# Kernel optimization log

Measured on AMD Instinct MI355X. Metric: run time of the kernel, lower is better.

The kernel has to match this reference:

```python
import jax, jax.numpy as jnp
import numpy as np

BINS = 100
MIN, MAX = 0.0, 1.0
DELTA = (MAX - MIN) / BINS
NORM = True
K = 2  # half-window: relu(delta - 0.5*(|dx|+|dy|)) is zero unless |x-c| < 2*delta per axis,
       # and centers are spaced delta apart, so only offsets -2..2 around the containing bin contribute.
BIG = 1e9  # sentinel distance for out-of-range bins -> zero weight


def setup_inputs() -> dict:
    key = jax.random.key(0)
    x = jax.random.uniform(key, (16, 131072, 2), dtype=jnp.float32)  # [B, N, 2] in [0,1)
    return {"x": x}


def reference(x):
    # Faithful to the torch double loop:
    #   counts[b,i,j] = sum_n relu(delta - 0.5*(|x[b,n,0]-c_i| + |x[b,n,1]-c_j|))
    # The triangular kernel has compact support, so each point touches at most a
    # 5x5 neighborhood of bins; compute those weights and scatter-add them.
    B, N, _ = x.shape
    centers = MIN + DELTA * (jnp.arange(BINS, dtype=x.dtype) + 0.5)  # [BINS]
    offs = jnp.arange(-K, K + 1)                                     # [5]

    idx = jnp.floor((x - MIN) / DELTA).astype(jnp.int32)             # [B,N,2] containing bin
    idx = jnp.clip(idx, 0, BINS - 1)
    nb = idx[..., None] + offs                                       # [B,N,2,5] candidate bins
    valid = (nb >= 0) & (nb < BINS)
    nbc = jnp.clip(nb, 0, BINS - 1)

    d = jnp.abs(x[..., None] - centers[nbc])                         # [B,N,2,5] per-axis L1 dist
    d = jnp.where(valid, d, BIG)                                     # kill out-of-range bins

    # combined 5x5 triangular weights per point
    w = jax.nn.relu(DELTA - 0.5 * (d[:, :, 0, :, None] + d[:, :, 1, None, :]))  # [B,N,5,5]

    ii = nbc[:, :, 0, :, None]                                       # [B,N,5,1]
    jj = nbc[:, :, 1, None, :]                                       # [B,N,1,5]
    flat = (jnp.arange(B, dtype=jnp.int32)[:, None, None, None] * (BINS * BINS)
            + ii * BINS + jj)                                        # [B,N,5,5]

    counts = jnp.zeros(B * BINS * BINS, dtype=x.dtype)
    counts = counts.at[flat.reshape(-1)].add(w.reshape(-1))
    counts = counts.reshape(B, BINS, BINS)

    if NORM:
        counts = counts / (counts.sum(axis=(1, 2), keepdims=True) + 1e-5)
    return counts
```

## Files before the change

### kernel.cpp

```cpp
#include <hip/hip_runtime.h>


#define BINS     100
#define NBINS2   (BINS * BINS)
#define NPOINTS  131072
#define NBATCH   16
#define PPB      32
#define CHUNK    (NPOINTS / PPB)
#define THREADS  1024
#define NPART    (NBATCH * PPB)
#define QSCALE   33554432.0f
#define QINV     (1.0 / 33554432.0)

__device__ __forceinline__ void accum_point_q(unsigned* lh, float x0, float x1) {
    int i0 = __float2int_rd(__fmul_rn(x0, 100.0f)); i0 = min(max(i0, 0), BINS - 1);
    int i1 = __float2int_rd(__fmul_rn(x1, 100.0f)); i1 = min(max(i1, 0), BINS - 1);
    const float fi0 = (float)i0, fi1 = (float)i1;
    const float c00 = __fmul_rn(0.01f, fi0 + 0.5f);
    const float c10 = __fmul_rn(0.01f, fi1 + 0.5f);
    const float e00 = fabsf(__fsub_rn(x0, c00));
    const float e10 = fabsf(__fsub_rn(x1, c10));
    float e0m = fabsf(__fsub_rn(x0, __fmul_rn(0.01f, fi0 - 0.5f)));
    float e0p = fabsf(__fsub_rn(x0, __fmul_rn(0.01f, fi0 + 1.5f)));
    float e1m = fabsf(__fsub_rn(x1, __fmul_rn(0.01f, fi1 - 0.5f)));
    float e1p = fabsf(__fsub_rn(x1, __fmul_rn(0.01f, fi1 + 1.5f)));
    e0m = (i0 > 0)        ? e0m : 1e9f;
    e0p = (i0 < BINS - 1) ? e0p : 1e9f;
    e1m = (i1 > 0)        ? e1m : 1e9f;
    e1p = (i1 < BINS - 1) ? e1p : 1e9f;
    const bool up0 = (x0 > c00), up1 = (x1 > c10);
    const int   f0  = up0 ? i0 + 2 : i0 - 2;
    const int   f1  = up1 ? i1 + 2 : i1 - 2;
    const float ff0 = up0 ? fi0 + 2.0f : fi0 - 2.0f;
    const float ff1 = up1 ? fi1 + 2.0f : fi1 - 2.0f;
    float e0f = fabsf(__fsub_rn(x0, __fmul_rn(0.01f, ff0 + 0.5f)));
    float e1f = fabsf(__fsub_rn(x1, __fmul_rn(0.01f, ff1 + 0.5f)));
    e0f = ((unsigned)f0 < (unsigned)BINS) ? e0f : 1e9f;
    e1f = ((unsigned)f1 < (unsigned)BINS) ? e1f : 1e9f;

    const int rm = max(i0 - 1, 0) * BINS;
    const int r0 = i0 * BINS;
    const int rp = min(i0 + 1, BINS - 1) * BINS;
    const int rf = min(max(f0, 0), BINS - 1) * BINS;
    const int cm = max(i1 - 1, 0);
    const int cc = i1;
    const int cp = min(i1 + 1, BINS - 1);
    const int cf = min(max(f1, 0), BINS - 1);

#define SITEU(EA, EB, ADDR) do {                                               \
        const float w_ = fmaxf(fmaf(-0.5f, __fadd_rn(EA, EB), 0.01f), 0.0f);   \
        atomicAdd(&lh[ADDR], (unsigned)fmaf(w_, QSCALE, 0.5f));                \
    } while (0)
#define SITEQ(EA, EB, ADDR) do {                                               \
        const float w_ = fmaf(-0.5f, __fadd_rn(EA, EB), 0.01f);                \
        if (w_ > 0.0f)                                                         \
            atomicAdd(&lh[ADDR], (unsigned)fmaf(w_, QSCALE, 0.5f));            \
    } while (0)
    SITEQ(e0m, e1m, rm + cm); SITEU(e0m, e10, rm + cc); SITEQ(e0m, e1p, rm + cp);
    SITEU(e00, e1m, r0 + cm); SITEU(e00, e10, r0 + cc); SITEU(e00, e1p, r0 + cp);
    SITEQ(e0p, e1m, rp + cm); SITEU(e0p, e10, rp + cc); SITEQ(e0p, e1p, rp + cp);
    SITEQ(e0f, e10, rf + cc);
    SITEQ(e00, e1f, r0 + cf);
#undef SITEU
#undef SITEQ
}

__global__ __launch_bounds__(THREADS) void hist_part_kernel(
    const float* __restrict__ x, unsigned* __restrict__ part,
    unsigned long long* __restrict__ totals)
{
    __shared__ __align__(16) unsigned lh[NBINS2];
    uint4* lh4 = (uint4*)lh;
    for (int i = threadIdx.x; i < NBINS2 / 4; i += THREADS)
        lh4[i] = make_uint4(0u, 0u, 0u, 0u);
    __syncthreads();

    const int b  = blockIdx.x / PPB;
    const int pb = blockIdx.x % PPB;
    const float4* __restrict__ xp = reinterpret_cast<const float4*>(
        x + (size_t)b * (NPOINTS * 2) + (size_t)pb * (CHUNK * 2));

    #pragma unroll
    for (int k = 0; k < (CHUNK / 2) / THREADS; ++k) {
        const float4 p = xp[threadIdx.x + k * THREADS];
        accum_point_q(lh, p.x, p.y);
        accum_point_q(lh, p.z, p.w);
    }
    __syncthreads();

    uint4* __restrict__ po4 = (uint4*)(part + (size_t)blockIdx.x * NBINS2);
    unsigned long long ts = 0ull;
    for (int i = threadIdx.x; i < NBINS2 / 4; i += THREADS) {
        const uint4 v = lh4[i];
        po4[i] = v;
        ts += (unsigned long long)v.x + v.y + v.z + v.w;
    }
    #pragma unroll
    for (int off = 32; off > 0; off >>= 1) ts += __shfl_down(ts, off, 64);
    if ((threadIdx.x & 63) == 0) atomicAdd(&totals[b], ts);
}

__global__ __launch_bounds__(1024) void reduce_norm_kernel(
    const unsigned* __restrict__ part, const unsigned long long* __restrict__ totals,
    float* __restrict__ out)
{
    const int b = blockIdx.x & 15;
    const int q = blockIdx.x >> 4;
    const int t = threadIdx.x;
    if (t < 1000) {
        const int bin = q * 1000 + t;
        const unsigned* __restrict__ pp = part + (size_t)b * PPB * NBINS2 + bin;
        unsigned long long s0 = 0ull, s1 = 0ull;
        #pragma unroll
        for (int p = 0; p < PPB; p += 2) {
            s0 += pp[(size_t)p       * NBINS2];
            s1 += pp[(size_t)(p + 1) * NBINS2];
        }
        const double T   = (double)totals[b];
        const double fac = QINV / (T * QINV + 1e-5);
        out[(size_t)b * NBINS2 + bin] = (float)((double)(s0 + s1) * fac);
    }
}

__device__ __forceinline__ void accum_point_f(float* lh, float x0, float x1) {
    int i0 = __float2int_rd(__fmul_rn(x0, 100.0f)); i0 = min(max(i0, 0), BINS - 1);
    int i1 = __float2int_rd(__fmul_rn(x1, 100.0f)); i1 = min(max(i1, 0), BINS - 1);
    const float fi0 = (float)i0, fi1 = (float)i1;
    const float c00 = __fmul_rn(0.01f, fi0 + 0.5f);
    const float c10 = __fmul_rn(0.01f, fi1 + 0.5f);
    const float e00 = fabsf(__fsub_rn(x0, c00));
    const float e10 = fabsf(__fsub_rn(x1, c10));
    float e0m = fabsf(__fsub_rn(x0, __fmul_rn(0.01f, fi0 - 0.5f)));
    float e0p = fabsf(__fsub_rn(x0, __fmul_rn(0.01f, fi0 + 1.5f)));
    float e1m = fabsf(__fsub_rn(x1, __fmul_rn(0.01f, fi1 - 0.5f)));
    float e1p = fabsf(__fsub_rn(x1, __fmul_rn(0.01f, fi1 + 1.5f)));
    e0m = (i0 > 0)        ? e0m : 1e9f;
    e0p = (i0 < BINS - 1) ? e0p : 1e9f;
    e1m = (i1 > 0)        ? e1m : 1e9f;
    e1p = (i1 < BINS - 1) ? e1p : 1e9f;
    const bool up0 = (x0 > c00), up1 = (x1 > c10);
    const int   f0  = up0 ? i0 + 2 : i0 - 2;
    const int   f1  = up1 ? i1 + 2 : i1 - 2;
    const float ff0 = up0 ? fi0 + 2.0f : fi0 - 2.0f;
    const float ff1 = up1 ? fi1 + 2.0f : fi1 - 2.0f;
    float e0f = fabsf(__fsub_rn(x0, __fmul_rn(0.01f, ff0 + 0.5f)));
    float e1f = fabsf(__fsub_rn(x1, __fmul_rn(0.01f, ff1 + 0.5f)));
    e0f = ((unsigned)f0 < (unsigned)BINS) ? e0f : 1e9f;
    e1f = ((unsigned)f1 < (unsigned)BINS) ? e1f : 1e9f;
    const int rm = max(i0 - 1, 0) * BINS;
    const int r0 = i0 * BINS;
    const int rp = min(i0 + 1, BINS - 1) * BINS;
    const int rf = min(max(f0, 0), BINS - 1) * BINS;
    const int cm = max(i1 - 1, 0);
    const int cc = i1;
    const int cp = min(i1 + 1, BINS - 1);
    const int cf = min(max(f1, 0), BINS - 1);
#define SITEF(EA, EB, ADDR) do {                                               \
        const float w_ = fmaf(-0.5f, __fadd_rn(EA, EB), 0.01f);                \
        if (w_ > 0.0f) unsafeAtomicAdd(&lh[ADDR], w_);                         \
    } while (0)
    SITEF(e0m, e1m, rm + cm); SITEF(e0m, e10, rm + cc); SITEF(e0m, e1p, rm + cp);
    SITEF(e00, e1m, r0 + cm); SITEF(e00, e10, r0 + cc); SITEF(e00, e1p, r0 + cp);
    SITEF(e0p, e1m, rp + cm); SITEF(e0p, e10, rp + cc); SITEF(e0p, e1p, rp + cp);
    SITEF(e0f, e10, rf + cc);
    SITEF(e00, e1f, r0 + cf);
#undef SITEF
}

__global__ __launch_bounds__(THREADS) void hist_accum_kernel(
    const float* __restrict__ x, float* __restrict__ out)
{
    __shared__ __align__(16) float lh[NBINS2];
    float4* lh4 = (float4*)lh;
    for (int i = threadIdx.x; i < NBINS2 / 4; i += THREADS)
        lh4[i] = make_float4(0.f, 0.f, 0.f, 0.f);
    __syncthreads();
    const int b  = blockIdx.x / PPB;
    const int pb = blockIdx.x % PPB;
    const float4* __restrict__ xp = reinterpret_cast<const float4*>(
        x + (size_t)b * (NPOINTS * 2) + (size_t)pb * (CHUNK * 2));
    #pragma unroll
    for (int k = 0; k < (CHUNK / 2) / THREADS; ++k) {
        const float4 p = xp[threadIdx.x + k * THREADS];
        accum_point_f(lh, p.x, p.y);
        accum_point_f(lh, p.z, p.w);
    }
    __syncthreads();
    float* __restrict__ ob = out + (size_t)b * NBINS2;
    for (int i = threadIdx.x; i < NBINS2; i += THREADS) {
        const float v = lh[i];
        if (v != 0.0f) unsafeAtomicAdd(&ob[i], v);
    }
}

__global__ __launch_bounds__(1024) void norm_kernel(float* __restrict__ out)
{
    const int b = blockIdx.x;
    float* __restrict__ h = out + (size_t)b * NBINS2;
    float local = 0.0f;
    for (int i = threadIdx.x; i < NBINS2; i += 1024) local += h[i];
    #pragma unroll
    for (int off = 32; off > 0; off >>= 1) local += __shfl_down(local, off, 64);
    __shared__ float wsum[16];
    __shared__ float sden;
    if ((threadIdx.x & 63) == 0) wsum[threadIdx.x >> 6] = local;
    __syncthreads();
    if (threadIdx.x == 0) {
        float tt = 0.f;
        #pragma unroll
        for (int i = 0; i < 16; ++i) tt += wsum[i];
        sden = __fadd_rn(tt, 1e-5f);
    }
    __syncthreads();
    const float den = sden;
    for (int i = threadIdx.x; i < 1024 * 10; i += 1024)
        if (i < NBINS2) h[i] = __fdiv_rn(h[i], den);
}

extern "C" void kernel_launch(void* const* d_in, const int* in_sizes, int n_in,
                              void* d_out, int out_size, void* d_ws, size_t ws_size,
                              hipStream_t stream) {
    (void)in_sizes; (void)n_in;
    const float* x = (const float*)d_in[0];
    float* out = (float*)d_out;

    const size_t need = 128 + (size_t)NPART * NBINS2 * sizeof(unsigned);
    if (ws_size >= need) {
        unsigned long long* totals = (unsigned long long*)d_ws;
        unsigned* part = (unsigned*)((char*)d_ws + 128);
        hipMemsetAsync(totals, 0, NBATCH * sizeof(unsigned long long), stream);
        hist_part_kernel<<<NPART, THREADS, 0, stream>>>(x, part, totals);
        reduce_norm_kernel<<<NBATCH * 10, 1024, 0, stream>>>(part, totals, out);
    } else {
        hipMemsetAsync(out, 0, (size_t)out_size * sizeof(float), stream);
        hist_accum_kernel<<<NPART, THREADS, 0, stream>>>(x, out);
        norm_kernel<<<NBATCH, 1024, 0, stream>>>(out);
    }
}
```

Measured before the change: 158.2 us.

## Merge per-block histograms with packed 64-bit global atomics instead of partial buffers

Each block now adds its shared-memory histogram straight into a per-batch global accumulator. It packs two adjacent 32-bit bins into one 64-bit atomic add and skips pairs that are zero. This drops the large per-block partial buffer, so there is no longer a full write and re-read of every block's histogram. The reduce kernel becomes a light vectorised scale-and-normalise pass. The cost is 32-way atomic contention per address, plus a small risk that a carry from the low 32-bit bin spills into its neighbour if a bin's quantised sum ever overflows.

Result: faster. 151.0 us (-4.5%).

```diff
diff --git a/kernel.cpp b/kernel.cpp
--- a/kernel.cpp
+++ b/kernel.cpp
@@ -3,6 +3,7 @@
 
 #define BINS     100
 #define NBINS2   (BINS * BINS)
+#define NPAIR    (NBINS2 / 2)
 #define NPOINTS  131072
 #define NBATCH   16
 #define PPB      32
@@ -66,7 +67,7 @@
 }
 
 __global__ __launch_bounds__(THREADS) void hist_part_kernel(
-    const float* __restrict__ x, unsigned* __restrict__ part,
+    const float* __restrict__ x, unsigned* __restrict__ accum,
     unsigned long long* __restrict__ totals)
 {
     __shared__ __align__(16) unsigned lh[NBINS2];
@@ -88,37 +89,36 @@
     }
     __syncthreads();
 
-    uint4* __restrict__ po4 = (uint4*)(part + (size_t)blockIdx.x * NBINS2);
+    const uint2* __restrict__ lh2 = (const uint2*)lh;
+    unsigned long long* __restrict__ acc2 =
+        (unsigned long long*)(accum + (size_t)b * NBINS2);
     unsigned long long ts = 0ull;
-    for (int i = threadIdx.x; i < NBINS2 / 4; i += THREADS) {
-        const uint4 v = lh4[i];
-        po4[i] = v;
-        ts += (unsigned long long)v.x + v.y + v.z + v.w;
+    for (int i = threadIdx.x; i < NPAIR; i += THREADS) {
+        const uint2 v = lh2[i];
+        const unsigned long long pk =
+            (unsigned long long)v.x | ((unsigned long long)v.y << 32);
+        if (pk) atomicAdd(&acc2[i], pk);
+        ts += (unsigned long long)v.x + v.y;
     }
     #pragma unroll
     for (int off = 32; off > 0; off >>= 1) ts += __shfl_down(ts, off, 64);
     if ((threadIdx.x & 63) == 0) atomicAdd(&totals[b], ts);
 }
 
-__global__ __launch_bounds__(1024) void reduce_norm_kernel(
-    const unsigned* __restrict__ part, const unsigned long long* __restrict__ totals,
-    float* __restrict__ out)
-{
-    const int b = blockIdx.x & 15;
-    const int q = blockIdx.x >> 4;
-    const int t = threadIdx.x;
-    if (t < 1000) {
-        const int bin = q * 1000 + t;
-        const unsigned* __restrict__ pp = part + (size_t)b * PPB * NBINS2 + bin;
-        unsigned long long s0 = 0ull, s1 = 0ull;
-        #pragma unroll
-        for (int p = 0; p < PPB; p += 2) {
-            s0 += pp[(size_t)p       * NBINS2];
-            s1 += pp[(size_t)(p + 1) * NBINS2];
-        }
-        const double T   = (double)totals[b];
-        const double fac = QINV / (T * QINV + 1e-5);
-        out[(size_t)b * NBINS2 + bin] = (float)((double)(s0 + s1) * fac);
+__global__ __launch_bounds__(256) void reduce_norm_kernel(
+    const uint4* __restrict__ accum4, const unsigned long long* __restrict__ totals,
+    float4* __restrict__ out4)
+{
+    const int b  = blockIdx.x / 10;
+    const int ch = blockIdx.x % 10;
+    const int t  = threadIdx.x;
+    if (t < 250) {
+        const int idx = b * (NBINS2 / 4) + ch * 250 + t;
+        const uint4 v = accum4[idx];
+        const double fac = QINV / ((double)totals[b] * QINV + 1e-5);
+        out4[idx] = make_float4(
+            (float)((double)v.x * fac), (float)((double)v.y * fac),
+            (float)((double)v.z * fac), (float)((double)v.w * fac));
     }
 }
 
@@ -213,8 +213,7 @@
     }
     __syncthreads();
     const float den = sden;
-    for (int i = threadIdx.x; i < 1024 * 10; i += 1024)
-        if (i < NBINS2) h[i] = __fdiv_rn(h[i], den);
+    for (int i = threadIdx.x; i < NBINS2; i += 1024) h[i] = __fdiv_rn(h[i], den);
 }
 
 extern "C" void kernel_launch(void* const* d_in, const int* in_sizes, int n_in,
@@ -224,13 +223,14 @@
     const float* x = (const float*)d_in[0];
     float* out = (float*)d_out;
 
-    const size_t need = 128 + (size_t)NPART * NBINS2 * sizeof(unsigned);
+    const size_t need = 128 + (size_t)NBATCH * NBINS2 * sizeof(unsigned);
     if (ws_size >= need) {
         unsigned long long* totals = (unsigned long long*)d_ws;
-        unsigned* part = (unsigned*)((char*)d_ws + 128);
-        hipMemsetAsync(totals, 0, NBATCH * sizeof(unsigned long long), stream);
-        hist_part_kernel<<<NPART, THREADS, 0, stream>>>(x, part, totals);
-        reduce_norm_kernel<<<NBATCH * 10, 1024, 0, stream>>>(part, totals, out);
+        unsigned* accum = (unsigned*)((char*)d_ws + 128);
+        hipMemsetAsync(d_ws, 0, need, stream);
+        hist_part_kernel<<<NPART, THREADS, 0, stream>>>(x, accum, totals);
+        reduce_norm_kernel<<<NBATCH * 10, 256, 0, stream>>>(
+            (const uint4*)accum, totals, (float4*)out);
     } else {
         hipMemsetAsync(out, 0, (size_t)out_size * sizeof(float), stream);
         hist_accum_kernel<<<NPART, THREADS, 0, stream>>>(x, out);
```
